# Kernel optimization log

Hardware: AMD Instinct MI355X
Metric: run time of the kernel (lower is better)

Reference implementation:

```python
import jax, jax.numpy as jnp
import numpy as np

N_NODES = 50000
N_EDGES = 800000
NODE_IN = 256
EDGE_OUT = 64
GLOBAL_IN = 128
NODE_OUT = 256
HIDDEN = 512
N_GRAPHS = 64


def setup_inputs() -> dict:
    key = jax.random.key(0)
    ks = jax.random.split(key, 8)
    x = jax.random.normal(ks[0], (N_NODES, NODE_IN), dtype=jnp.float32)
    edge_index = jax.random.randint(ks[1], (2, N_EDGES), 0, N_NODES, dtype=jnp.int64)
    edge_attr = jax.random.normal(ks[2], (N_EDGES, EDGE_OUT), dtype=jnp.float32)
    u = jax.random.normal(ks[3], (N_GRAPHS, GLOBAL_IN), dtype=jnp.float32)
    batch = jnp.sort(jax.random.randint(ks[4], (N_NODES,), 0, N_GRAPHS, dtype=jnp.int64))
    in_dim = NODE_IN + EDGE_OUT + GLOBAL_IN
    # MLP params (torch nn.Linear default init: U(-1/sqrt(fan_in), 1/sqrt(fan_in)))
    b1s = 1.0 / np.sqrt(in_dim)
    b2s = 1.0 / np.sqrt(HIDDEN)
    W1 = jax.random.uniform(ks[5], (in_dim, HIDDEN), dtype=jnp.float32, minval=-b1s, maxval=b1s)
    b1 = jnp.zeros((HIDDEN,), dtype=jnp.float32)
    W2 = jax.random.uniform(ks[6], (HIDDEN, NODE_OUT), dtype=jnp.float32, minval=-b2s, maxval=b2s)
    b2 = jnp.zeros((NODE_OUT,), dtype=jnp.float32)
    return {"x": x, "edge_index": edge_index, "edge_attr": edge_attr, "u": u,
            "batch": batch, "W1": W1, "b1": b1, "W2": W2, "b2": b2}


def reference(x, edge_index, edge_attr, u, batch, W1, b1, W2, b2):
    n = x.shape[0]
    src = edge_index[0]
    # scatter_mean(edge_attr, src, dim=0, dim_size=n)
    sums = jax.ops.segment_sum(edge_attr, src, num_segments=n)          # [N, E_out]
    counts = jax.ops.segment_sum(jnp.ones((edge_attr.shape[0],), edge_attr.dtype),
                                 src, num_segments=n)                   # [N]
    edge_attr_agg = sums / jnp.maximum(counts, 1.0)[:, None]
    u_expanded = u[batch]                                               # [N, G_in]
    combined = jnp.concatenate([x, edge_attr_agg, u_expanded], axis=1)  # [N, 448]
    h = jax.nn.relu(combined @ W1 + b1)                                 # [N, H]
    return h @ W2 + b2                                                  # [N, N_out]
```

## Files before the change

### kernel.cpp

```cpp
#include <hip/hip_runtime.h>
#include <hip/hip_bf16.h>
#include <stdint.h>

#define NN 50000
#define NE 800000
#define NODE_IN 256
#define EDGE_OUT 64
#define GLOBAL_IN 128
#define NODE_OUT 256
#define HIDDEN 512
#define K1 320
#define N_GRAPHS 64
#define MAXDEG 64

typedef __attribute__((ext_vector_type(8))) short bf16x8;
typedef __attribute__((ext_vector_type(4))) float f32x4;
typedef __attribute__((ext_vector_type(4))) unsigned short us4;

__device__ __forceinline__ unsigned short f2bf(float x) {
    union { float f; unsigned int u; } c; c.f = x;
    unsigned int u = c.u;
    unsigned int r = (u + 0x7FFFu + ((u >> 16) & 1u)) >> 16;
    return (unsigned short)r;
}

#define GLD_LDS(gp, lp) __builtin_amdgcn_global_load_lds( \
    (const __attribute__((address_space(1))) unsigned int*)(gp), \
    (__attribute__((address_space(3))) unsigned int*)(lp), 16, 0, 0)

#define PREP_W1 (HIDDEN * K1)
#define PREP_W2 (PREP_W1 + NODE_OUT * HIDDEN)
#define PREP_G  (PREP_W2 + N_GRAPHS * HIDDEN)
#define PREP_Z  (PREP_G + NN)
__global__ __launch_bounds__(256)
void prep(const float* __restrict__ W1, const float* __restrict__ W2,
          const float* __restrict__ u, const float* __restrict__ b1,
          unsigned short* __restrict__ W1T, unsigned short* __restrict__ W2T,
          float* __restrict__ G, int* __restrict__ cnt)
{
    int idx = blockIdx.x * 256 + threadIdx.x;
    if (idx < PREP_W1) {
        int n = idx / K1, k = idx - n * K1;
        W1T[idx] = f2bf(W1[(size_t)k * HIDDEN + n]);
    } else if (idx < PREP_W2) {
        int j = idx - PREP_W1;
        int n = j / HIDDEN, k = j - n * HIDDEN;
        W2T[j] = f2bf(W2[(size_t)k * NODE_OUT + n]);
    } else if (idx < PREP_G) {
        int j = idx - PREP_W2;
        int g = j >> 9, col = j & 511;
        const float* up = u + (size_t)g * GLOBAL_IN;
        float acc = b1[col];
        #pragma unroll 4
        for (int k = 0; k < GLOBAL_IN; ++k)
            acc += up[k] * W1[(size_t)(K1 + k) * HIDDEN + col];
        G[j] = acc;
    } else if (idx < PREP_Z) {
        cnt[idx - PREP_G] = 0;
    }
}

__global__ __launch_bounds__(256)
void fillx(const int* __restrict__ src, int* __restrict__ cnt,
           int* __restrict__ perm, const float* __restrict__ x,
           unsigned short* __restrict__ comb)
{
    const int gs = gridDim.x * 256;
    for (int e = blockIdx.x * 256 + threadIdx.x; e < NE; e += gs) {
        int s = src[e];
        int pos = atomicAdd(&cnt[s], 1);
        if (pos < MAXDEG) perm[(size_t)s * MAXDEG + pos] = e;
    }
    for (int q = blockIdx.x * 256 + threadIdx.x; q < NN * 64; q += gs) {
        int node = q >> 6, lane = q & 63;
        const float4 v = *(const float4*)(x + (size_t)node * NODE_IN + lane * 4);
        us4 o = { f2bf(v.x), f2bf(v.y), f2bf(v.z), f2bf(v.w) };
        *(us4*)(comb + (size_t)node * K1 + lane * 4) = o;
    }
}

__global__ __launch_bounds__(256)
void seg(const float* __restrict__ edge_attr, const int* __restrict__ perm,
         const int* __restrict__ cnt, unsigned short* __restrict__ comb)
{
    int node = blockIdx.x * 4 + (threadIdx.x >> 6);
    if (node >= NN) return;
    int lane = threadIdx.x & 63;
    int g = lane >> 4, f = (lane & 15) * 4;
    int c = cnt[node];
    int cc = c < MAXDEG ? c : MAXDEG;
    const int* pbase = perm + (size_t)node * MAXDEG;
    int eperm = pbase[lane];
    float4 a0 = make_float4(0.f, 0.f, 0.f, 0.f);
    float4 a1 = make_float4(0.f, 0.f, 0.f, 0.f);
    const int nb = (cc + 7) >> 3;
    for (int kb = 0; kb < nb; ++kb) {
        int i0 = (kb << 3) + g;
        int i1 = i0 + 4;
        int e0 = __shfl(eperm, i0, 64);
        int e1 = __shfl(eperm, i1, 64);
        if (i0 < cc) {
            const float4 v0 = *(const float4*)(edge_attr + (size_t)e0 * EDGE_OUT + f);
            a0.x += v0.x; a0.y += v0.y; a0.z += v0.z; a0.w += v0.w;
        }
        if (i1 < cc) {
            const float4 v1 = *(const float4*)(edge_attr + (size_t)e1 * EDGE_OUT + f);
            a1.x += v1.x; a1.y += v1.y; a1.z += v1.z; a1.w += v1.w;
        }
    }
    float4 acc = make_float4(a0.x + a1.x, a0.y + a1.y, a0.z + a1.z, a0.w + a1.w);
    #pragma unroll
    for (int off = 16; off < 64; off <<= 1) {
        acc.x += __shfl_xor(acc.x, off, 64);
        acc.y += __shfl_xor(acc.y, off, 64);
        acc.z += __shfl_xor(acc.z, off, 64);
        acc.w += __shfl_xor(acc.w, off, 64);
    }
    if (g == 0) {
        float inv = 1.0f / fmaxf((float)c, 1.0f);
        us4 o = { f2bf(acc.x * inv), f2bf(acc.y * inv),
                  f2bf(acc.z * inv), f2bf(acc.w * inv) };
        *(us4*)(comb + (size_t)node * K1 + NODE_IN + f) = o;
    }
}

template<int EPI>
__global__ __launch_bounds__(256)
void gemm_bt_128(const unsigned short* __restrict__ A,
                 const unsigned short* __restrict__ B,
                 const float* __restrict__ bias,
                 const int* __restrict__ batch,
                 void* __restrict__ Cv,
                 int M, int N, int K)
{
    __shared__ unsigned short lA[128 * 64];
    __shared__ unsigned short lB[128 * 64];
    const int tid = threadIdx.x;
    const int w = tid >> 6, l = tid & 63;

    const int nwg  = gridDim.x * gridDim.y;
    const int orig = blockIdx.x + gridDim.x * blockIdx.y;
    const int q = nwg >> 3, r = nwg & 7;
    const int xcd = orig & 7, sidx = orig >> 3;
    const int wg = (xcd < r ? xcd * (q + 1) : r * (q + 1) + (xcd - r) * q) + sidx;
    const int m0 = (wg / gridDim.x) * 128;
    const int n0 = (wg % gridDim.x) * 128;

    const int wr = w >> 1, wc = w & 1;

    f32x4 acc[4][4] = {};

    const unsigned short* pAs[4];
    const unsigned short* pBs[4];
    #pragma unroll
    for (int i = 0; i < 4; ++i) {
        int c = tid + i * 256;
        int row = c >> 3;
        int kg = ((c & 7) ^ (row & 7)) * 8;
        int gr = m0 + row; if (gr >= M) gr = M - 1;
        pAs[i] = A + (size_t)gr * K + kg;
        pBs[i] = B + (size_t)(n0 + row) * K + kg;
    }

    for (int k0 = 0; k0 < K; k0 += 64) {
        #pragma unroll
        for (int i = 0; i < 4; ++i)
            GLD_LDS(pAs[i] + k0, &lA[(size_t)(tid + i * 256) * 8]);
        #pragma unroll
        for (int i = 0; i < 4; ++i)
            GLD_LDS(pBs[i] + k0, &lB[(size_t)(tid + i * 256) * 8]);
        __syncthreads();

        #pragma unroll
        for (int kk = 0; kk < 2; ++kk) {
            bf16x8 af[4], bfr[4];
            #pragma unroll
            for (int m = 0; m < 4; ++m) {
                int ar = wr * 64 + m * 16 + (l & 15);
                int gran = (kk * 4 + (l >> 4)) ^ (ar & 7);
                af[m] = *(const bf16x8*)&lA[ar * 64 + gran * 8];
            }
            #pragma unroll
            for (int n = 0; n < 4; ++n) {
                int br = wc * 64 + n * 16 + (l & 15);
                int gran = (kk * 4 + (l >> 4)) ^ (br & 7);
                bfr[n] = *(const bf16x8*)&lB[br * 64 + gran * 8];
            }
            #pragma unroll
            for (int m = 0; m < 4; ++m)
                #pragma unroll
                for (int n = 0; n < 4; ++n)
                    acc[m][n] = __builtin_amdgcn_mfma_f32_16x16x32_bf16(af[m], bfr[n], acc[m][n], 0, 0, 0);
        }
        __syncthreads();
    }

    const int cbase = n0 + wc * 64 + (l & 15);
    const int rbase = m0 + wr * 64 + ((l >> 4) << 2);
    if (EPI == 0) {
        unsigned short* C = (unsigned short*)Cv;
        #pragma unroll
        for (int m = 0; m < 4; ++m) {
            #pragma unroll
            for (int j = 0; j < 4; ++j) {
                int row = rbase + m * 16 + j;
                if (row < M) {
                    const float* grow = bias + (size_t)batch[row] * HIDDEN;
                    #pragma unroll
                    for (int n = 0; n < 4; ++n) {
                        int c = cbase + n * 16;
                        float v = acc[m][n][j] + grow[c];
                        v = fmaxf(v, 0.0f);
                        C[(size_t)row * N + c] = f2bf(v);
                    }
                }
            }
        }
    } else {
        float* C = (float*)Cv;
        #pragma unroll
        for (int m = 0; m < 4; ++m) {
            #pragma unroll
            for (int j = 0; j < 4; ++j) {
                int row = rbase + m * 16 + j;
                if (row < M) {
                    #pragma unroll
                    for (int n = 0; n < 4; ++n) {
                        int c = cbase + n * 16;
                        C[(size_t)row * N + c] = acc[m][n][j] + bias[c];
                    }
                }
            }
        }
    }
}

extern "C" void kernel_launch(void* const* d_in, const int* in_sizes, int n_in,
                              void* d_out, int out_size, void* d_ws, size_t ws_size,
                              hipStream_t stream)
{
    const float* x         = (const float*)d_in[0];
    const int*   src       = (const int*)d_in[1];
    const float* edge_attr = (const float*)d_in[2];
    const float* u         = (const float*)d_in[3];
    const int*   batch     = (const int*)d_in[4];
    const float* W1        = (const float*)d_in[5];
    const float* b1        = (const float*)d_in[6];
    const float* W2        = (const float*)d_in[7];
    const float* b2        = (const float*)d_in[8];
    float* out = (float*)d_out;

    char* ws = (char*)d_ws;
    int*            cnt    = (int*)(ws);
    int*            perm   = (int*)(ws + 200704);
    unsigned short* comb   = (unsigned short*)(ws + 13000704);
    unsigned short* W1T    = (unsigned short*)(ws + 45000704);
    unsigned short* W2T    = (unsigned short*)(ws + 45328384);
    float*          G      = (float*)(ws + 45590528);
    unsigned short* h      = (unsigned short*)(ws + 45721600);

    prep<<<(PREP_Z + 255) / 256, 256, 0, stream>>>(W1, W2, u, b1, W1T, W2T, G, cnt);

    fillx<<<2048, 256, 0, stream>>>(src, cnt, perm, x, comb);

    seg<<<(NN + 3) / 4, 256, 0, stream>>>(edge_attr, perm, cnt, comb);

    gemm_bt_128<0><<<dim3(HIDDEN / 128, (NN + 127) / 128), 256, 0, stream>>>(
        comb, W1T, G, batch, h, NN, HIDDEN, K1);
    gemm_bt_128<1><<<dim3(NODE_OUT / 128, (NN + 127) / 128), 256, 0, stream>>>(
        h, W2T, b2, nullptr, out, NN, NODE_OUT, HIDDEN);
}
```

Before: 206.4 us.

## Fuse all stages into a persistent cooperative kernel with grid syncs

Replaces the five separate launches with one cooperative kernel that runs prep, edge bucketing, x conversion, segment mean, and both GEMMs, separated by grid-wide barriers. Each block owns one 128-row M tile and loops over N tiles. The goal is to remove launch gaps and inter-kernel tails. In exchange, GEMM work is split into only 391 coarse blocks, which can load-imbalance across CUs, and grid syncs add cost. A fallback to the multi-kernel path remains if the cooperative launch fails.

Result: slower. 448.8 us (+117.4%).

```diff
diff --git a/kernel.cpp b/kernel.cpp
--- a/kernel.cpp
+++ b/kernel.cpp
@@ -1,6 +1,9 @@
 #include <hip/hip_runtime.h>
 #include <hip/hip_bf16.h>
+#include <hip/hip_cooperative_groups.h>
 #include <stdint.h>
+
+namespace cg = cooperative_groups;
 
 #define NN 50000
 #define NE 800000
@@ -12,6 +15,8 @@
 #define K1 320
 #define N_GRAPHS 64
 #define MAXDEG 64
+#define MT 391
+#define NBLK MT
 
 typedef __attribute__((ext_vector_type(8))) short bf16x8;
 typedef __attribute__((ext_vector_type(4))) float f32x4;
@@ -31,14 +36,13 @@
 #define PREP_W1 (HIDDEN * K1)
 #define PREP_W2 (PREP_W1 + NODE_OUT * HIDDEN)
 #define PREP_G  (PREP_W2 + N_GRAPHS * HIDDEN)
-#define PREP_Z  (PREP_G + NN)
-__global__ __launch_bounds__(256)
-void prep(const float* __restrict__ W1, const float* __restrict__ W2,
-          const float* __restrict__ u, const float* __restrict__ b1,
-          unsigned short* __restrict__ W1T, unsigned short* __restrict__ W2T,
-          float* __restrict__ G, int* __restrict__ cnt)
-{
-    int idx = blockIdx.x * 256 + threadIdx.x;
+
+__device__ __forceinline__ void prep_body(int idx,
+    const float* __restrict__ W1, const float* __restrict__ W2,
+    const float* __restrict__ u, const float* __restrict__ b1,
+    unsigned short* __restrict__ W1T, unsigned short* __restrict__ W2T,
+    float* __restrict__ G)
+{
     if (idx < PREP_W1) {
         int n = idx / K1, k = idx - n * K1;
         W1T[idx] = f2bf(W1[(size_t)k * HIDDEN + n]);
@@ -55,37 +59,14 @@
         for (int k = 0; k < GLOBAL_IN; ++k)
             acc += up[k] * W1[(size_t)(K1 + k) * HIDDEN + col];
         G[j] = acc;
-    } else if (idx < PREP_Z) {
-        cnt[idx - PREP_G] = 0;
-    }
-}
-
-__global__ __launch_bounds__(256)
-void fillx(const int* __restrict__ src, int* __restrict__ cnt,
-           int* __restrict__ perm, const float* __restrict__ x,
-           unsigned short* __restrict__ comb)
-{
-    const int gs = gridDim.x * 256;
-    for (int e = blockIdx.x * 256 + threadIdx.x; e < NE; e += gs) {
-        int s = src[e];
-        int pos = atomicAdd(&cnt[s], 1);
-        if (pos < MAXDEG) perm[(size_t)s * MAXDEG + pos] = e;
-    }
-    for (int q = blockIdx.x * 256 + threadIdx.x; q < NN * 64; q += gs) {
-        int node = q >> 6, lane = q & 63;
-        const float4 v = *(const float4*)(x + (size_t)node * NODE_IN + lane * 4);
-        us4 o = { f2bf(v.x), f2bf(v.y), f2bf(v.z), f2bf(v.w) };
-        *(us4*)(comb + (size_t)node * K1 + lane * 4) = o;
-    }
-}
-
-__global__ __launch_bounds__(256)
-void seg(const float* __restrict__ edge_attr, const int* __restrict__ perm,
-         const int* __restrict__ cnt, unsigned short* __restrict__ comb)
-{
-    int node = blockIdx.x * 4 + (threadIdx.x >> 6);
-    if (node >= NN) return;
-    int lane = threadIdx.x & 63;
+    }
+}
+
+__device__ __forceinline__ void seg_body(int node, int tid,
+    const float* __restrict__ edge_attr, const int* __restrict__ perm,
+    const int* __restrict__ cnt, unsigned short* __restrict__ comb)
+{
+    int lane = tid & 63;
     int g = lane >> 4, f = (lane & 15) * 4;
     int c = cnt[node];
     int cc = c < MAXDEG ? c : MAXDEG;
@@ -125,27 +106,15 @@
 }
 
 template<int EPI>
-__global__ __launch_bounds__(256)
-void gemm_bt_128(const unsigned short* __restrict__ A,
-                 const unsigned short* __restrict__ B,
-                 const float* __restrict__ bias,
-                 const int* __restrict__ batch,
-                 void* __restrict__ Cv,
-                 int M, int N, int K)
+__device__ __forceinline__ void gemm_tile(
+    const unsigned short* __restrict__ A, const unsigned short* __restrict__ B,
+    const float* __restrict__ bias, const int* __restrict__ batch,
+    void* __restrict__ Cv, int m0, int n0, int M, int N, int K)
 {
     __shared__ unsigned short lA[128 * 64];
     __shared__ unsigned short lB[128 * 64];
     const int tid = threadIdx.x;
     const int w = tid >> 6, l = tid & 63;
-
-    const int nwg  = gridDim.x * gridDim.y;
-    const int orig = blockIdx.x + gridDim.x * blockIdx.y;
-    const int q = nwg >> 3, r = nwg & 7;
-    const int xcd = orig & 7, sidx = orig >> 3;
-    const int wg = (xcd < r ? xcd * (q + 1) : r * (q + 1) + (xcd - r) * q) + sidx;
-    const int m0 = (wg / gridDim.x) * 128;
-    const int n0 = (wg % gridDim.x) * 128;
-
     const int wr = w >> 1, wc = w & 1;
 
     f32x4 acc[4][4] = {};
@@ -235,6 +204,107 @@
     }
 }
 
+__global__ __launch_bounds__(256, 2)
+void mega(const float* __restrict__ x, const int* __restrict__ src,
+          const float* __restrict__ edge_attr, const float* __restrict__ u,
+          const int* __restrict__ batch, const float* __restrict__ W1,
+          const float* __restrict__ b1, const float* __restrict__ W2,
+          const float* __restrict__ b2, float* __restrict__ out,
+          int* __restrict__ cnt, int* __restrict__ perm,
+          unsigned short* __restrict__ comb, unsigned short* __restrict__ W1T,
+          unsigned short* __restrict__ W2T, float* __restrict__ G,
+          unsigned short* __restrict__ h)
+{
+    cg::grid_group grid = cg::this_grid();
+    const int tid = threadIdx.x;
+    const int bid = blockIdx.x;
+    const int gs = NBLK * 256;
+    const int gid = bid * 256 + tid;
+
+    for (int idx = gid; idx < PREP_G; idx += gs)
+        prep_body(idx, W1, W2, u, b1, W1T, W2T, G);
+    for (int e = gid; e < NE; e += gs) {
+        int s = src[e];
+        int pos = atomicAdd(&cnt[s], 1);
+        if (pos < MAXDEG) perm[(size_t)s * MAXDEG + pos] = e;
+    }
+    for (int q = gid; q < NN * 64; q += gs) {
+        int node = q >> 6, lane = q & 63;
+        const float4 v = *(const float4*)(x + (size_t)node * NODE_IN + lane * 4);
+        us4 o = { f2bf(v.x), f2bf(v.y), f2bf(v.z), f2bf(v.w) };
+        *(us4*)(comb + (size_t)node * K1 + lane * 4) = o;
+    }
+    grid.sync();
+
+    for (int nb = bid; nb < NN / 4; nb += NBLK) {
+        int node = nb * 4 + (tid >> 6);
+        seg_body(node, tid, edge_attr, perm, cnt, comb);
+    }
+    grid.sync();
+
+    #pragma unroll 1
+    for (int ni = 0; ni < 4; ++ni)
+        gemm_tile<0>(comb, W1T, G, batch, h, bid * 128, ni * 128, NN, HIDDEN, K1);
+    grid.sync();
+
+    #pragma unroll 1
+    for (int ni = 0; ni < 2; ++ni)
+        gemm_tile<1>(h, W2T, b2, nullptr, out, bid * 128, ni * 128, NN, NODE_OUT, HIDDEN);
+}
+
+__global__ __launch_bounds__(256)
+void k_prep(const float* __restrict__ W1, const float* __restrict__ W2,
+            const float* __restrict__ u, const float* __restrict__ b1,
+            unsigned short* __restrict__ W1T, unsigned short* __restrict__ W2T,
+            float* __restrict__ G)
+{
+    int idx = blockIdx.x * 256 + threadIdx.x;
+    if (idx < PREP_G) prep_body(idx, W1, W2, u, b1, W1T, W2T, G);
+}
+
+__global__ __launch_bounds__(256)
+void k_fillx(const int* __restrict__ src, int* __restrict__ cnt,
+             int* __restrict__ perm, const float* __restrict__ x,
+             unsigned short* __restrict__ comb)
+{
+    const int gs = gridDim.x * 256;
+    for (int e = blockIdx.x * 256 + threadIdx.x; e < NE; e += gs) {
+        int s = src[e];
+        int pos = atomicAdd(&cnt[s], 1);
+        if (pos < MAXDEG) perm[(size_t)s * MAXDEG + pos] = e;
+    }
+    for (int q = blockIdx.x * 256 + threadIdx.x; q < NN * 64; q += gs) {
+        int node = q >> 6, lane = q & 63;
+        const float4 v = *(const float4*)(x + (size_t)node * NODE_IN + lane * 4);
+        us4 o = { f2bf(v.x), f2bf(v.y), f2bf(v.z), f2bf(v.w) };
+        *(us4*)(comb + (size_t)node * K1 + lane * 4) = o;
+    }
+}
+
+__global__ __launch_bounds__(256)
+void k_seg(const float* __restrict__ edge_attr, const int* __restrict__ perm,
+           const int* __restrict__ cnt, unsigned short* __restrict__ comb)
+{
+    int node = blockIdx.x * 4 + (threadIdx.x >> 6);
+    if (node < NN) seg_body(node, threadIdx.x, edge_attr, perm, cnt, comb);
+}
+
+template<int EPI>
+__global__ __launch_bounds__(256)
+void k_gemm(const unsigned short* __restrict__ A, const unsigned short* __restrict__ B,
+            const float* __restrict__ bias, const int* __restrict__ batch,
+            void* __restrict__ Cv, int M, int N, int K)
+{
+    const int nwg  = gridDim.x * gridDim.y;
+    const int orig = blockIdx.x + gridDim.x * blockIdx.y;
+    const int q = nwg >> 3, r = nwg & 7;
+    const int xcd = orig & 7, sidx = orig >> 3;
+    const int wg = (xcd < r ? xcd * (q + 1) : r * (q + 1) + (xcd - r) * q) + sidx;
+    const int m0 = (wg / gridDim.x) * 128;
+    const int n0 = (wg % gridDim.x) * 128;
+    gemm_tile<EPI>(A, B, bias, batch, Cv, m0, n0, M, N, K);
+}
+
 extern "C" void kernel_launch(void* const* d_in, const int* in_sizes, int n_in,
                               void* d_out, int out_size, void* d_ws, size_t ws_size,
                               hipStream_t stream)
@@ -259,14 +329,22 @@
     float*          G      = (float*)(ws + 45590528);
     unsigned short* h      = (unsigned short*)(ws + 45721600);
 
-    prep<<<(PREP_Z + 255) / 256, 256, 0, stream>>>(W1, W2, u, b1, W1T, W2T, G, cnt);
-
-    fillx<<<2048, 256, 0, stream>>>(src, cnt, perm, x, comb);
-
-    seg<<<(NN + 3) / 4, 256, 0, stream>>>(edge_attr, perm, cnt, comb);
-
-    gemm_bt_128<0><<<dim3(HIDDEN / 128, (NN + 127) / 128), 256, 0, stream>>>(
-        comb, W1T, G, batch, h, NN, HIDDEN, K1);
-    gemm_bt_128<1><<<dim3(NODE_OUT / 128, (NN + 127) / 128), 256, 0, stream>>>(
-        h, W2T, b2, nullptr, out, NN, NODE_OUT, HIDDEN);
-}
+    hipMemsetAsync(cnt, 0, 200000, stream);
+
+    void* kargs[] = { (void*)&x, (void*)&src, (void*)&edge_attr, (void*)&u,
+                      (void*)&batch, (void*)&W1, (void*)&b1, (void*)&W2,
+                      (void*)&b2, (void*)&out, (void*)&cnt, (void*)&perm,
+                      (void*)&comb, (void*)&W1T, (void*)&W2T, (void*)&G,
+                      (void*)&h };
+    hipError_t err = hipLaunchCooperativeKernel((const void*)mega, dim3(NBLK),
+                                                dim3(256), kargs, 0, stream);
+    if (err != hipSuccess) {
+        k_prep<<<(PREP_G + 255) / 256, 256, 0, stream>>>(W1, W2, u, b1, W1T, W2T, G);
+        k_fillx<<<2048, 256, 0, stream>>>(src, cnt, perm, x, comb);
+        k_seg<<<(NN + 3) / 4, 256, 0, stream>>>(edge_attr, perm, cnt, comb);
+        k_gemm<0><<<dim3(HIDDEN / 128, (NN + 127) / 128), 256, 0, stream>>>(
+            comb, W1T, G, batch, h, NN, HIDDEN, K1);
+        k_gemm<1><<<dim3(NODE_OUT / 128, (NN + 127) / 128), 256, 0, stream>>>(
+            h, W2T, b2, nullptr, out, NN, NODE_OUT, HIDDEN);
+    }
+}
```
